# Optimization experiments

Measured on AMD Instinct MI355X. Metric: run time of the kernel, lower is better.

Reference implementation:

```python
import jax, jax.numpy as jnp
import numpy as np

N = 50000   # nodes
E = 800000  # edges (avg degree 16)
D = 64      # in_feat
OUT = 64    # out_feat


def _layernorm(x, gamma, beta, eps=1e-5):
    m = jnp.mean(x, axis=-1, keepdims=True)
    v = jnp.mean((x - m) ** 2, axis=-1, keepdims=True)  # biased var, as torch LayerNorm
    return (x - m) * jax.lax.rsqrt(v + eps) * gamma + beta


def setup_inputs() -> dict:
    key = jax.random.key(0)
    ks = jax.random.split(key, 6)
    s1 = 1.0 / np.sqrt(D)
    s2 = 1.0 / np.sqrt(2 * D)
    return {
        "x": jax.random.normal(ks[0], (N, D), dtype=jnp.float32),
        "edge_index": jax.random.randint(ks[1], (2, E), 0, N, dtype=jnp.int64),
        "W1a": jax.random.normal(ks[2], (D, D), dtype=jnp.float32) * s1,
        "W1b": jax.random.normal(ks[3], (D, D), dtype=jnp.float32) * s1,
        "gamma1": jnp.ones((D,), jnp.float32),
        "beta1": jnp.zeros((D,), jnp.float32),
        "w": jnp.ones((D,), jnp.float32),
        "gamma2": jnp.ones((D,), jnp.float32),
        "beta2": jnp.zeros((D,), jnp.float32),
        "W2a": jax.random.normal(ks[4], (D, 2 * D), dtype=jnp.float32) * s2,
        "W2b": jax.random.normal(ks[5], (OUT, D), dtype=jnp.float32) * s1,
    }


def reference(x, edge_index, W1a, W1b, gamma1, beta1, w, gamma2, beta2, W2a, W2b):
    row, col = edge_index[0], edge_index[1]
    n = x.shape[0]
    # gather -> MLP1 (two bias-free linears with ReLU)
    msg = x[row]                                        # [E, D]
    msg = jax.nn.relu(msg @ W1a.T) @ W1b.T              # [E, D]
    # scatter_mean over destination nodes
    s = jax.ops.segment_sum(msg, col, num_segments=n)   # [N, D]
    cnt = jax.ops.segment_sum(jnp.ones((col.shape[0],), x.dtype), col, num_segments=n)
    agg = s / jnp.maximum(cnt, 1.0)[:, None]
    agg = _layernorm(agg, gamma1, beta1)
    # repulsion + residual + LayerNorm
    fx = _layernorm(x + (x - agg) * w, gamma2, beta2)
    # concat -> MLP2
    h = jnp.concatenate([fx, agg], axis=1)              # [N, 2D]
    return jax.nn.relu(h @ W2a.T) @ W2b.T               # [N, OUT]
```

## Files before the change

### kernel.cpp

```cpp
#include <hip/hip_runtime.h>
#include <hip/hip_bf16.h>

#define NN 50000
#define NE 800000
#define CAP 48
#define BINS 784
#define BPAD 1024
#define P1B 391
#define CHUNK 2048
#define MLPB 768
#define SUPT 782

typedef short v8s __attribute__((ext_vector_type(8)));
typedef float v4f __attribute__((ext_vector_type(4)));
#define MFMA16(a, b, c) __builtin_amdgcn_mfma_f32_16x16x32_bf16(a, b, c, 0, 0, 0)

__device__ __forceinline__ float bfu2f(unsigned short u) {
    union { unsigned int i; float f; } v; v.i = ((unsigned int)u) << 16; return v.f;
}
__device__ __forceinline__ unsigned short f2bf_rne(float f) {
    union { float f; unsigned int i; } v; v.f = f;
    unsigned int x = v.i;
    unsigned int r = x + 0x7fffu + ((x >> 16) & 1u);
    return (unsigned short)(r >> 16);
}
__device__ __forceinline__ v8s fragf32(const float* p) {
    float4 u = ((const float4*)p)[0];
    float4 v = ((const float4*)p)[1];
    v8s r;
    r[0] = (short)f2bf_rne(u.x); r[1] = (short)f2bf_rne(u.y);
    r[2] = (short)f2bf_rne(u.z); r[3] = (short)f2bf_rne(u.w);
    r[4] = (short)f2bf_rne(v.x); r[5] = (short)f2bf_rne(v.y);
    r[6] = (short)f2bf_rne(v.z); r[7] = (short)f2bf_rne(v.w);
    return r;
}
__device__ __forceinline__ v8s fragbf(const unsigned short* p) {
    union { uint4 u; v8s s; } t; t.u = *((const uint4*)p); return t.s;
}
__device__ __forceinline__ v4f vzero() { v4f z; z[0]=0.f; z[1]=0.f; z[2]=0.f; z[3]=0.f; return z; }

__global__ __launch_bounds__(256) void p1fat_k(const int* __restrict__ ei,
                                               const float* __restrict__ x,
                                               const float* __restrict__ W1a,
                                               const float* __restrict__ W1b,
                                               unsigned int* __restrict__ chunkbuf,
                                               unsigned short* __restrict__ histT,
                                               unsigned short* __restrict__ y) {
    __shared__ unsigned int smem[6912];
    int t = threadIdx.x;
    if (blockIdx.x < P1B) {
        unsigned int* hcnt = smem;
        unsigned int* sst  = smem + BPAD;
        unsigned int* data = smem + 2 * BPAD;
        unsigned int* scan = data;
        int p = blockIdx.x;
        int e0 = p * CHUNK;
        int e1 = e0 + CHUNK; if (e1 > NE) e1 = NE;
        int ne = e1 - e0;
        bool i64 = ((ei[1] | ei[3] | ei[5] | ei[7]) == 0);
        for (int i = t; i < BPAD; i += 256) hcnt[i] = 0;
        __syncthreads();
        unsigned int packed[8];
#pragma unroll
        for (int i = 0; i < 8; ++i) {
            int e = e0 + t + 256 * i;
            unsigned int pk = 0xFFFFFFFFu;
            if (e < e1) {
                int col = i64 ? ei[2 * (NE + e)] : ei[NE + e];
                int row = i64 ? ei[2 * e]        : ei[e];
                pk = ((unsigned int)col << 16) | (unsigned int)row;
                atomicAdd(&hcnt[col >> 6], 1u);
            }
            packed[i] = pk;
        }
        __syncthreads();
        unsigned int v0 = hcnt[4 * t], v1 = hcnt[4 * t + 1];
        unsigned int v2 = hcnt[4 * t + 2], v3 = hcnt[4 * t + 3];
        unsigned int tsum = v0 + v1 + v2 + v3;
        scan[t] = tsum;
        __syncthreads();
        for (int off = 1; off < 256; off <<= 1) {
            unsigned int a = (t >= off) ? scan[t - off] : 0;
            __syncthreads();
            scan[t] += a;
            __syncthreads();
        }
        {
            unsigned int base = scan[t] - tsum;
            unsigned int s0 = base, s1 = base + v0, s2 = s1 + v1, s3 = s2 + v2;
            hcnt[4 * t] = s0; hcnt[4 * t + 1] = s1;
            hcnt[4 * t + 2] = s2; hcnt[4 * t + 3] = s3;
            sst[4 * t] = s0; sst[4 * t + 1] = s1;
            sst[4 * t + 2] = s2; sst[4 * t + 3] = s3;
        }
        __syncthreads();
#pragma unroll
        for (int i = 0; i < 8; ++i) {
            unsigned int pk = packed[i];
            if (pk != 0xFFFFFFFFu) {
                unsigned int pos = atomicAdd(&hcnt[pk >> 22], 1u);
                data[pos] = pk;
            }
        }
        __syncthreads();
        unsigned int* cb = chunkbuf + (size_t)p * CHUNK;
        for (int i = t; i < ne; i += 256) cb[i] = data[i];
        for (int i = t; i < BINS; i += 256)
            histT[i * P1B + p] = (unsigned short)sst[i];
        return;
    }
    unsigned short* wa  = (unsigned short*)smem;
    unsigned short* wb  = wa + 64 * 72;
    unsigned short* h1s = wb + 64 * 72;
    for (int i = t; i < 64 * 64; i += 256) {
        int r = i >> 6, c = i & 63;
        wa[r * 72 + c] = f2bf_rne(W1a[i]);
        wb[r * 72 + c] = f2bf_rne(W1b[i]);
    }
    __syncthreads();
    int w = t >> 6, l = t & 63;
    int lm = l & 15, lq = l >> 4;
    for (int st = blockIdx.x - P1B; st < SUPT; st += MLPB) {
        int nb = st * 64;
        int arow = nb + w * 16 + lm;
        int arc = arow < NN ? arow : NN - 1;
        const float* xr = x + (size_t)arc * 64;
        v8s a0 = fragf32(xr + lq * 8);
        v8s a1 = fragf32(xr + 32 + lq * 8);
        v4f acc[4];
#pragma unroll
        for (int jt = 0; jt < 4; ++jt) acc[jt] = vzero();
#pragma unroll
        for (int jt = 0; jt < 4; ++jt) {
            const unsigned short* wr = &wa[(jt * 16 + lm) * 72];
            acc[jt] = MFMA16(a0, fragbf(wr + lq * 8), acc[jt]);
            acc[jt] = MFMA16(a1, fragbf(wr + 32 + lq * 8), acc[jt]);
        }
#pragma unroll
        for (int jt = 0; jt < 4; ++jt)
#pragma unroll
            for (int r = 0; r < 4; ++r)
                h1s[(w * 16 + lq * 4 + r) * 72 + jt * 16 + lm] = f2bf_rne(fmaxf(acc[jt][r], 0.0f));
        __syncthreads();
        v8s c0 = fragbf(&h1s[(w * 16 + lm) * 72 + lq * 8]);
        v8s c1 = fragbf(&h1s[(w * 16 + lm) * 72 + 32 + lq * 8]);
        v4f acc2[4];
#pragma unroll
        for (int jt = 0; jt < 4; ++jt) acc2[jt] = vzero();
#pragma unroll
        for (int jt = 0; jt < 4; ++jt) {
            const unsigned short* wr = &wb[(jt * 16 + lm) * 72];
            acc2[jt] = MFMA16(c0, fragbf(wr + lq * 8), acc2[jt]);
            acc2[jt] = MFMA16(c1, fragbf(wr + 32 + lq * 8), acc2[jt]);
        }
#pragma unroll
        for (int jt = 0; jt < 4; ++jt)
#pragma unroll
            for (int r = 0; r < 4; ++r) {
                int n = nb + w * 16 + lq * 4 + r;
                if (n < NN) y[(size_t)n * 64 + jt * 16 + lm] = f2bf_rne(acc2[jt][r]);
            }
        __syncthreads();
    }
}

__global__ __launch_bounds__(256) void p2_k(const unsigned int* __restrict__ chunkbuf,
                                            const unsigned short* __restrict__ histT,
                                            unsigned short* __restrict__ bucket1,
                                            int* __restrict__ cnt) {
    __shared__ unsigned int cl[64];
    __shared__ unsigned short dl[64 * CAP];
    __shared__ unsigned int scan[256];
    __shared__ unsigned short sstart[P1B + 1];
    __shared__ unsigned short base[P1B + 1];
    int t = threadIdx.x;
    int b = blockIdx.x;
    int c0 = b << 6;
    for (int i = t; i < 64; i += 256) cl[i] = 0;
    for (int i = t; i < 64 * CAP / 2; i += 256) ((unsigned int*)dl)[i] = 0;
    unsigned int l0 = 0, l1 = 0;
    {
        int s0 = 2 * t, s1 = 2 * t + 1;
        if (s0 < P1B) {
            unsigned int st = histT[b * P1B + s0];
            int ne = NE - s0 * CHUNK; if (ne > CHUNK) ne = CHUNK;
            unsigned int en = (b == BINS - 1) ? (unsigned int)ne : histT[(b + 1) * P1B + s0];
            l0 = en - st;
            sstart[s0] = (unsigned short)st;
        }
        if (s1 < P1B) {
            unsigned int st = histT[b * P1B + s1];
            int ne = NE - s1 * CHUNK; if (ne > CHUNK) ne = CHUNK;
            unsigned int en = (b == BINS - 1) ? (unsigned int)ne : histT[(b + 1) * P1B + s1];
            l1 = en - st;
            sstart[s1] = (unsigned short)st;
        }
    }
    unsigned int psum = l0 + l1;
    scan[t] = psum;
    __syncthreads();
    for (int off = 1; off < 256; off <<= 1) {
        unsigned int a = (t >= off) ? scan[t - off] : 0;
        __syncthreads();
        scan[t] += a;
        __syncthreads();
    }
    {
        unsigned int excl = scan[t] - psum;
        if (2 * t < P1B)     base[2 * t]     = (unsigned short)excl;
        if (2 * t + 1 < P1B) base[2 * t + 1] = (unsigned short)(excl + l0);
    }
    __syncthreads();
    int tot = (int)scan[255];
    for (int k = t; k < tot; k += 256) {
        int lo = 0, hi = P1B - 1;
#pragma unroll
        for (int it = 0; it < 9; ++it) {
            int mid = (lo + hi + 1) >> 1;
            if ((int)base[mid] <= k) lo = mid; else hi = mid - 1;
        }
        int idx = (int)sstart[lo] + (k - (int)base[lo]);
        unsigned int d = chunkbuf[(size_t)lo * CHUNK + idx];
        int c = (int)(d >> 16) - c0;
        unsigned int slot = atomicAdd(&cl[c], 1u);
        if (slot < CAP) dl[c * CAP + slot] = (unsigned short)(d & 0xffffu);
    }
    __syncthreads();
    for (int i = t; i < 64; i += 256)
        if (c0 + i < NN) cnt[c0 + i] = (int)cl[i];
    uint4* dst = (uint4*)(bucket1 + (size_t)c0 * CAP);
    const uint4* src = (const uint4*)dl;
    for (int i = t; i < 64 * CAP / 8; i += 256) dst[i] = src[i];
}

__device__ __forceinline__ float wsum64(float v) {
#pragma unroll
    for (int o = 32; o > 0; o >>= 1) v += __shfl_xor(v, o, 64);
    return v;
}
__device__ __forceinline__ void ln_store(float s0, float s1, int tdeg, int n, int p, int j, int f0,
                                         const float* __restrict__ x,
                                         const float* __restrict__ g1, const float* __restrict__ b1,
                                         const float* __restrict__ wrep,
                                         const float* __restrict__ g2, const float* __restrict__ b2,
                                         unsigned short* __restrict__ h) {
    float inv = 1.0f / (float)(tdeg > 1 ? tdeg : 1);
    float a0 = s0 * inv, a1 = s1 * inv;
    float m = wsum64(a0 + a1) * (1.0f / 128.0f);
    float d0 = a0 - m, d1 = a1 - m;
    float var = wsum64(d0 * d0 + d1 * d1) * (1.0f / 128.0f);
    float r = rsqrtf(var + 1e-5f);
    float2 g1v = *(const float2*)(g1 + f0);
    float2 b1v = *(const float2*)(b1 + f0);
    a0 = d0 * r * g1v.x + b1v.x;
    a1 = d1 * r * g1v.y + b1v.y;
    float2 xv = *(const float2*)(x + (size_t)n * 64 + f0);
    float2 wv = *(const float2*)(wrep + f0);
    float t0 = xv.x + (xv.x - a0) * wv.x;
    float t1 = xv.y + (xv.y - a1) * wv.y;
    float m2 = wsum64(t0 + t1) * (1.0f / 128.0f);
    float e0 = t0 - m2, e1 = t1 - m2;
    float var2 = wsum64(e0 * e0 + e1 * e1) * (1.0f / 128.0f);
    float r2 = rsqrtf(var2 + 1e-5f);
    float2 g2v = *(const float2*)(g2 + f0);
    float2 b2v = *(const float2*)(b2 + f0);
    float fx0 = e0 * r2 * g2v.x + b2v.x;
    float fx1 = e1 * r2 * g2v.y + b2v.y;
    unsigned* hw = (unsigned*)(h + (size_t)n * 128);
    if (p == 0) hw[j]      = (unsigned)f2bf_rne(fx0) | ((unsigned)f2bf_rne(fx1) << 16);
    else        hw[32 + j] = (unsigned)f2bf_rne(a0)  | ((unsigned)f2bf_rne(a1)  << 16);
}
__global__ __launch_bounds__(256) void gathernorm_k(const int* __restrict__ cnt,
                                                    const unsigned short* __restrict__ bucket1,
                                                    const unsigned short* __restrict__ y,
                                                    const float* __restrict__ x,
                                                    const float* __restrict__ g1, const float* __restrict__ b1,
                                                    const float* __restrict__ wrep,
                                                    const float* __restrict__ g2, const float* __restrict__ b2,
                                                    unsigned short* __restrict__ h) {
    int n0 = blockIdx.x * 8 + (threadIdx.x >> 6) * 2;
    if (n0 >= NN) return;
    int n1 = n0 + 1;
    int n1c = n1 < NN ? n1 : n0;
    int l = threadIdx.x & 63;
    int p = l >> 5;
    int j = l & 31;
    int f0 = 2 * j;
    int dA = cnt[n0], dB = cnt[n1c];
    int eA = dA < CAP ? dA : CAP;
    int eB = dB < CAP ? dB : CAP;
    const uint4* bpA = (const uint4*)(bucket1 + (size_t)n0 * CAP);
    const uint4* bpB = (const uint4*)(bucket1 + (size_t)n1c * CAP);
    uint4 qA[6], qB[6];
#pragma unroll
    for (int i = 0; i < 6; ++i) { qA[i] = bpA[i]; qB[i] = bpB[i]; }
    float sA0 = 0.f, sA1 = 0.f, sB0 = 0.f, sB1 = 0.f;
#pragma unroll
    for (int c = 0; c < 6; ++c) {
        bool cA = c * 8 < eA, cB = c * 8 < eB;
        if (cA | cB) {
            unsigned wA[4] = { qA[c].x, qA[c].y, qA[c].z, qA[c].w };
            unsigned wB[4] = { qB[c].x, qB[c].y, qB[c].z, qB[c].w };
#pragma unroll
            for (int i = 0; i < 4; ++i) {
                int e = c * 8 + 2 * i + p;
                int idA = (int)((wA[i] >> (p * 16)) & 0xffffu);
                int idB = (int)((wB[i] >> (p * 16)) & 0xffffu);
                unsigned uA = *(const unsigned*)(y + (size_t)idA * 64 + f0);
                unsigned uB = *(const unsigned*)(y + (size_t)idB * 64 + f0);
                bool okA = cA && e < eA, okB = cB && e < eB;
                sA0 += okA ? bfu2f((unsigned short)(uA & 0xffffu)) : 0.0f;
                sA1 += okA ? bfu2f((unsigned short)(uA >> 16)) : 0.0f;
                sB0 += okB ? bfu2f((unsigned short)(uB & 0xffffu)) : 0.0f;
                sB1 += okB ? bfu2f((unsigned short)(uB >> 16)) : 0.0f;
            }
        }
    }
    sA0 += __shfl_xor(sA0, 32, 64);
    sA1 += __shfl_xor(sA1, 32, 64);
    sB0 += __shfl_xor(sB0, 32, 64);
    sB1 += __shfl_xor(sB1, 32, 64);
    ln_store(sA0, sA1, dA, n0, p, j, f0, x, g1, b1, wrep, g2, b2, h);
    if (n1 < NN)
        ln_store(sB0, sB1, dB, n1, p, j, f0, x, g1, b1, wrep, g2, b2, h);
}

__global__ __launch_bounds__(256) void mlp2_k(const unsigned short* hin,
                                              const float* __restrict__ W2a,
                                              const float* __restrict__ W2b,
                                              float* out) {
    __shared__ unsigned short sm2[64 * 136 + 64 * 72 + 64 * 72];
    unsigned short* wa2 = sm2;
    unsigned short* wb2 = wa2 + 64 * 136;
    unsigned short* t2s = wb2 + 64 * 72;
    int t = threadIdx.x;
    for (int i = t; i < 64 * 128; i += 256) {
        int r = i >> 7, c = i & 127;
        wa2[r * 136 + c] = f2bf_rne(W2a[i]);
    }
    for (int i = t; i < 64 * 64; i += 256) {
        int r = i >> 6, c = i & 63;
        wb2[r * 72 + c] = f2bf_rne(W2b[i]);
    }
    __syncthreads();
    int w = t >> 6, l = t & 63;
    int lm = l & 15, lq = l >> 4;
    for (int st = blockIdx.x; st < SUPT; st += MLPB) {
        int nb = st * 64;
        int arow = nb + w * 16 + lm;
        int arc = arow < NN ? arow : NN - 1;
        const unsigned short* fr = hin + (size_t)arc * 128;
        v8s a0 = fragbf(fr + lq * 8);
        v8s a1 = fragbf(fr + 32 + lq * 8);
        v8s a2 = fragbf(fr + 64 + lq * 8);
        v8s a3 = fragbf(fr + 96 + lq * 8);
        v4f acc[4];
#pragma unroll
        for (int jt = 0; jt < 4; ++jt) acc[jt] = vzero();
#pragma unroll
        for (int jt = 0; jt < 4; ++jt) {
            const unsigned short* wr = &wa2[(jt * 16 + lm) * 136];
            acc[jt] = MFMA16(a0, fragbf(wr + lq * 8), acc[jt]);
            acc[jt] = MFMA16(a1, fragbf(wr + 32 + lq * 8), acc[jt]);
            acc[jt] = MFMA16(a2, fragbf(wr + 64 + lq * 8), acc[jt]);
            acc[jt] = MFMA16(a3, fragbf(wr + 96 + lq * 8), acc[jt]);
        }
#pragma unroll
        for (int jt = 0; jt < 4; ++jt)
#pragma unroll
            for (int r = 0; r < 4; ++r)
                t2s[(w * 16 + lq * 4 + r) * 72 + jt * 16 + lm] = f2bf_rne(fmaxf(acc[jt][r], 0.0f));
        __syncthreads();
        v8s c0 = fragbf(&t2s[(w * 16 + lm) * 72 + lq * 8]);
        v8s c1 = fragbf(&t2s[(w * 16 + lm) * 72 + 32 + lq * 8]);
        v4f acc2[4];
#pragma unroll
        for (int jt = 0; jt < 4; ++jt) acc2[jt] = vzero();
#pragma unroll
        for (int jt = 0; jt < 4; ++jt) {
            const unsigned short* wr = &wb2[(jt * 16 + lm) * 72];
            acc2[jt] = MFMA16(c0, fragbf(wr + lq * 8), acc2[jt]);
            acc2[jt] = MFMA16(c1, fragbf(wr + 32 + lq * 8), acc2[jt]);
        }
#pragma unroll
        for (int jt = 0; jt < 4; ++jt)
#pragma unroll
            for (int r = 0; r < 4; ++r) {
                int n = nb + w * 16 + lq * 4 + r;
                if (n < NN) out[(size_t)n * 64 + jt * 16 + lm] = acc2[jt][r];
            }
        __syncthreads();
    }
}

extern "C" void kernel_launch(void* const* d_in, const int* in_sizes, int n_in,
                              void* d_out, int out_size, void* d_ws, size_t ws_size,
                              hipStream_t stream) {
    const float* x   = (const float*)d_in[0];
    const int*   ei  = (const int*)d_in[1];
    const float* W1a = (const float*)d_in[2];
    const float* W1b = (const float*)d_in[3];
    const float* g1  = (const float*)d_in[4];
    const float* b1  = (const float*)d_in[5];
    const float* w   = (const float*)d_in[6];
    const float* g2  = (const float*)d_in[7];
    const float* b2  = (const float*)d_in[8];
    const float* W2a = (const float*)d_in[9];
    const float* W2b = (const float*)d_in[10];

    char* ws = (char*)d_ws;
    unsigned short* y        = (unsigned short*)(ws + 0);
    unsigned int*   chunkbuf = (unsigned int*)(ws + 6400000);
    unsigned short* histT    = (unsigned short*)(ws + 9603072);
    unsigned short* bucket1  = (unsigned short*)(ws + 10216160);
    int*            cnt      = (int*)(ws + 15033056);

    p1fat_k<<<P1B + MLPB, 256, 0, stream>>>(ei, x, W1a, W1b, chunkbuf, histT, y);
    p2_k<<<BINS, 256, 0, stream>>>(chunkbuf, histT, bucket1, cnt);
    gathernorm_k<<<(NN + 7) / 8, 256, 0, stream>>>(cnt, bucket1, y, x,
                                                   g1, b1, w, g2, b2, (unsigned short*)d_out);
    mlp2_k<<<MLPB, 256, 0, stream>>>((const unsigned short*)d_out, W2a, W2b, (float*)d_out);
    (void)in_sizes; (void)n_in; (void)out_size; (void)ws_size;
}
```

Baseline: 138.7 us.

## Fuse bucket scatter, gather-normalize and MLP2 into one kernel over 16-node bins

Shrinks the histogram bins from 64 to 16 destination nodes (3125 bins, bank-padded in shared memory) and transposes histT to a per-chunk row layout. Merges p2_k, gathernorm_k and mlp2_k into a single kernel in which each block buckets its 16 nodes' edges into shared memory, gathers and layer-normalizes them, and runs the MLP2 MFMAs directly from LDS. This removes two launches and the global round-trips through bucket1/cnt and the bf16 h buffer. In exchange every block re-converts the full W2a/W2b weights to bf16 and runs a per-block scan over all 391 chunks, across about four times as many blocks.

```diff
diff --git a/kernel.cpp b/kernel.cpp
--- a/kernel.cpp
+++ b/kernel.cpp
@@ -4,12 +4,13 @@
 #define NN 50000
 #define NE 800000
 #define CAP 48
-#define BINS 784
-#define BPAD 1024
+#define BINS 3125
+#define HROW 3126
 #define P1B 391
 #define CHUNK 2048
 #define MLPB 768
 #define SUPT 782
+#define HIDX(b) ((b) + ((b) >> 4))
 
 typedef short v8s __attribute__((ext_vector_type(8)));
 typedef float v4f __attribute__((ext_vector_type(4)));
@@ -46,19 +47,19 @@
                                                unsigned int* __restrict__ chunkbuf,
                                                unsigned short* __restrict__ histT,
                                                unsigned short* __restrict__ y) {
-    __shared__ unsigned int smem[6912];
+    __shared__ __align__(16) unsigned int smem[8448];
     int t = threadIdx.x;
     if (blockIdx.x < P1B) {
-        unsigned int* hcnt = smem;
-        unsigned int* sst  = smem + BPAD;
-        unsigned int* data = smem + 2 * BPAD;
-        unsigned int* scan = data;
-        int p = blockIdx.x;
-        int e0 = p * CHUNK;
+        unsigned int*   hcnt  = smem;
+        unsigned short* sst16 = (unsigned short*)(smem + 4352);
+        unsigned int*   data  = smem + 4352 + 2048;
+        unsigned int*   scan  = data;
+        int pc = blockIdx.x;
+        int e0 = pc * CHUNK;
         int e1 = e0 + CHUNK; if (e1 > NE) e1 = NE;
         int ne = e1 - e0;
         bool i64 = ((ei[1] | ei[3] | ei[5] | ei[7]) == 0);
-        for (int i = t; i < BPAD; i += 256) hcnt[i] = 0;
+        for (int i = t; i < 4352; i += 256) hcnt[i] = 0;
         __syncthreads();
         unsigned int packed[8];
 #pragma unroll
@@ -69,14 +70,14 @@
                 int col = i64 ? ei[2 * (NE + e)] : ei[NE + e];
                 int row = i64 ? ei[2 * e]        : ei[e];
                 pk = ((unsigned int)col << 16) | (unsigned int)row;
-                atomicAdd(&hcnt[col >> 6], 1u);
+                atomicAdd(&hcnt[HIDX(col >> 4)], 1u);
             }
             packed[i] = pk;
         }
         __syncthreads();
-        unsigned int v0 = hcnt[4 * t], v1 = hcnt[4 * t + 1];
-        unsigned int v2 = hcnt[4 * t + 2], v3 = hcnt[4 * t + 3];
-        unsigned int tsum = v0 + v1 + v2 + v3;
+        unsigned int vv[16], tsum = 0;
+#pragma unroll
+        for (int k = 0; k < 16; ++k) { vv[k] = hcnt[HIDX(16 * t + k)]; tsum += vv[k]; }
         scan[t] = tsum;
         __syncthreads();
         for (int off = 1; off < 256; off <<= 1) {
@@ -86,27 +87,30 @@
             __syncthreads();
         }
         {
-            unsigned int base = scan[t] - tsum;
-            unsigned int s0 = base, s1 = base + v0, s2 = s1 + v1, s3 = s2 + v2;
-            hcnt[4 * t] = s0; hcnt[4 * t + 1] = s1;
-            hcnt[4 * t + 2] = s2; hcnt[4 * t + 3] = s3;
-            sst[4 * t] = s0; sst[4 * t + 1] = s1;
-            sst[4 * t + 2] = s2; sst[4 * t + 3] = s3;
+            unsigned int run = scan[t] - tsum;
+#pragma unroll
+            for (int k = 0; k < 16; ++k) {
+                int bb = 16 * t + k;
+                hcnt[HIDX(bb)] = run;
+                sst16[bb] = (unsigned short)run;
+                run += vv[k];
+            }
         }
         __syncthreads();
 #pragma unroll
         for (int i = 0; i < 8; ++i) {
             unsigned int pk = packed[i];
             if (pk != 0xFFFFFFFFu) {
-                unsigned int pos = atomicAdd(&hcnt[pk >> 22], 1u);
+                unsigned int pos = atomicAdd(&hcnt[HIDX(pk >> 20)], 1u);
                 data[pos] = pk;
             }
         }
         __syncthreads();
-        unsigned int* cb = chunkbuf + (size_t)p * CHUNK;
+        unsigned int* cb = chunkbuf + (size_t)pc * CHUNK;
         for (int i = t; i < ne; i += 256) cb[i] = data[i];
-        for (int i = t; i < BINS; i += 256)
-            histT[i * P1B + p] = (unsigned short)sst[i];
+        unsigned short* hrow = histT + (size_t)pc * HROW;
+        for (int i = t; i < BINS; i += 256) hrow[i] = sst16[i];
+        if (t == 0) hrow[BINS] = (unsigned short)ne;
         return;
     }
     unsigned short* wa  = (unsigned short*)smem;
@@ -164,75 +168,6 @@
     }
 }
 
-__global__ __launch_bounds__(256) void p2_k(const unsigned int* __restrict__ chunkbuf,
-                                            const unsigned short* __restrict__ histT,
-                                            unsigned short* __restrict__ bucket1,
-                                            int* __restrict__ cnt) {
-    __shared__ unsigned int cl[64];
-    __shared__ unsigned short dl[64 * CAP];
-    __shared__ unsigned int scan[256];
-    __shared__ unsigned short sstart[P1B + 1];
-    __shared__ unsigned short base[P1B + 1];
-    int t = threadIdx.x;
-    int b = blockIdx.x;
-    int c0 = b << 6;
-    for (int i = t; i < 64; i += 256) cl[i] = 0;
-    for (int i = t; i < 64 * CAP / 2; i += 256) ((unsigned int*)dl)[i] = 0;
-    unsigned int l0 = 0, l1 = 0;
-    {
-        int s0 = 2 * t, s1 = 2 * t + 1;
-        if (s0 < P1B) {
-            unsigned int st = histT[b * P1B + s0];
-            int ne = NE - s0 * CHUNK; if (ne > CHUNK) ne = CHUNK;
-            unsigned int en = (b == BINS - 1) ? (unsigned int)ne : histT[(b + 1) * P1B + s0];
-            l0 = en - st;
-            sstart[s0] = (unsigned short)st;
-        }
-        if (s1 < P1B) {
-            unsigned int st = histT[b * P1B + s1];
-            int ne = NE - s1 * CHUNK; if (ne > CHUNK) ne = CHUNK;
-            unsigned int en = (b == BINS - 1) ? (unsigned int)ne : histT[(b + 1) * P1B + s1];
-            l1 = en - st;
-            sstart[s1] = (unsigned short)st;
-        }
-    }
-    unsigned int psum = l0 + l1;
-    scan[t] = psum;
-    __syncthreads();
-    for (int off = 1; off < 256; off <<= 1) {
-        unsigned int a = (t >= off) ? scan[t - off] : 0;
-        __syncthreads();
-        scan[t] += a;
-        __syncthreads();
-    }
-    {
-        unsigned int excl = scan[t] - psum;
-        if (2 * t < P1B)     base[2 * t]     = (unsigned short)excl;
-        if (2 * t + 1 < P1B) base[2 * t + 1] = (unsigned short)(excl + l0);
-    }
-    __syncthreads();
-    int tot = (int)scan[255];
-    for (int k = t; k < tot; k += 256) {
-        int lo = 0, hi = P1B - 1;
-#pragma unroll
-        for (int it = 0; it < 9; ++it) {
-            int mid = (lo + hi + 1) >> 1;
-            if ((int)base[mid] <= k) lo = mid; else hi = mid - 1;
-        }
-        int idx = (int)sstart[lo] + (k - (int)base[lo]);
-        unsigned int d = chunkbuf[(size_t)lo * CHUNK + idx];
-        int c = (int)(d >> 16) - c0;
-        unsigned int slot = atomicAdd(&cl[c], 1u);
-        if (slot < CAP) dl[c * CAP + slot] = (unsigned short)(d & 0xffffu);
-    }
-    __syncthreads();
-    for (int i = t; i < 64; i += 256)
-        if (c0 + i < NN) cnt[c0 + i] = (int)cl[i];
-    uint4* dst = (uint4*)(bucket1 + (size_t)c0 * CAP);
-    const uint4* src = (const uint4*)dl;
-    for (int i = t; i < 64 * CAP / 8; i += 256) dst[i] = src[i];
-}
-
 __device__ __forceinline__ float wsum64(float v) {
 #pragma unroll
     for (int o = 32; o > 0; o >>= 1) v += __shfl_xor(v, o, 64);
@@ -243,7 +178,7 @@
                                          const float* __restrict__ g1, const float* __restrict__ b1,
                                          const float* __restrict__ wrep,
                                          const float* __restrict__ g2, const float* __restrict__ b2,
-                                         unsigned short* __restrict__ h) {
+                                         unsigned short* hrow) {
     float inv = 1.0f / (float)(tdeg > 1 ? tdeg : 1);
     float a0 = s0 * inv, a1 = s1 * inv;
     float m = wsum64(a0 + a1) * (1.0f / 128.0f);
@@ -266,74 +201,34 @@
     float2 b2v = *(const float2*)(b2 + f0);
     float fx0 = e0 * r2 * g2v.x + b2v.x;
     float fx1 = e1 * r2 * g2v.y + b2v.y;
-    unsigned* hw = (unsigned*)(h + (size_t)n * 128);
+    unsigned* hw = (unsigned*)hrow;
     if (p == 0) hw[j]      = (unsigned)f2bf_rne(fx0) | ((unsigned)f2bf_rne(fx1) << 16);
     else        hw[32 + j] = (unsigned)f2bf_rne(a0)  | ((unsigned)f2bf_rne(a1)  << 16);
 }
-__global__ __launch_bounds__(256) void gathernorm_k(const int* __restrict__ cnt,
-                                                    const unsigned short* __restrict__ bucket1,
-                                                    const unsigned short* __restrict__ y,
-                                                    const float* __restrict__ x,
-                                                    const float* __restrict__ g1, const float* __restrict__ b1,
-                                                    const float* __restrict__ wrep,
-                                                    const float* __restrict__ g2, const float* __restrict__ b2,
-                                                    unsigned short* __restrict__ h) {
-    int n0 = blockIdx.x * 8 + (threadIdx.x >> 6) * 2;
-    if (n0 >= NN) return;
-    int n1 = n0 + 1;
-    int n1c = n1 < NN ? n1 : n0;
-    int l = threadIdx.x & 63;
-    int p = l >> 5;
-    int j = l & 31;
-    int f0 = 2 * j;
-    int dA = cnt[n0], dB = cnt[n1c];
-    int eA = dA < CAP ? dA : CAP;
-    int eB = dB < CAP ? dB : CAP;
-    const uint4* bpA = (const uint4*)(bucket1 + (size_t)n0 * CAP);
-    const uint4* bpB = (const uint4*)(bucket1 + (size_t)n1c * CAP);
-    uint4 qA[6], qB[6];
-#pragma unroll
-    for (int i = 0; i < 6; ++i) { qA[i] = bpA[i]; qB[i] = bpB[i]; }
-    float sA0 = 0.f, sA1 = 0.f, sB0 = 0.f, sB1 = 0.f;
-#pragma unroll
-    for (int c = 0; c < 6; ++c) {
-        bool cA = c * 8 < eA, cB = c * 8 < eB;
-        if (cA | cB) {
-            unsigned wA[4] = { qA[c].x, qA[c].y, qA[c].z, qA[c].w };
-            unsigned wB[4] = { qB[c].x, qB[c].y, qB[c].z, qB[c].w };
-#pragma unroll
-            for (int i = 0; i < 4; ++i) {
-                int e = c * 8 + 2 * i + p;
-                int idA = (int)((wA[i] >> (p * 16)) & 0xffffu);
-                int idB = (int)((wB[i] >> (p * 16)) & 0xffffu);
-                unsigned uA = *(const unsigned*)(y + (size_t)idA * 64 + f0);
-                unsigned uB = *(const unsigned*)(y + (size_t)idB * 64 + f0);
-                bool okA = cA && e < eA, okB = cB && e < eB;
-                sA0 += okA ? bfu2f((unsigned short)(uA & 0xffffu)) : 0.0f;
-                sA1 += okA ? bfu2f((unsigned short)(uA >> 16)) : 0.0f;
-                sB0 += okB ? bfu2f((unsigned short)(uB & 0xffffu)) : 0.0f;
-                sB1 += okB ? bfu2f((unsigned short)(uB >> 16)) : 0.0f;
-            }
-        }
-    }
-    sA0 += __shfl_xor(sA0, 32, 64);
-    sA1 += __shfl_xor(sA1, 32, 64);
-    sB0 += __shfl_xor(sB0, 32, 64);
-    sB1 += __shfl_xor(sB1, 32, 64);
-    ln_store(sA0, sA1, dA, n0, p, j, f0, x, g1, b1, wrep, g2, b2, h);
-    if (n1 < NN)
-        ln_store(sB0, sB1, dB, n1, p, j, f0, x, g1, b1, wrep, g2, b2, h);
-}
-
-__global__ __launch_bounds__(256) void mlp2_k(const unsigned short* hin,
+
+__global__ __launch_bounds__(256) void p2gm_k(const unsigned int* __restrict__ chunkbuf,
+                                              const unsigned short* __restrict__ histT,
+                                              const unsigned short* __restrict__ y,
+                                              const float* __restrict__ x,
+                                              const float* __restrict__ g1, const float* __restrict__ b1,
+                                              const float* __restrict__ wrep,
+                                              const float* __restrict__ g2, const float* __restrict__ b2,
                                               const float* __restrict__ W2a,
                                               const float* __restrict__ W2b,
-                                              float* out) {
-    __shared__ unsigned short sm2[64 * 136 + 64 * 72 + 64 * 72];
-    unsigned short* wa2 = sm2;
+                                              float* __restrict__ out) {
+    __shared__ __align__(16) unsigned int k2s[9368];
+    unsigned short* wa2 = (unsigned short*)k2s;
     unsigned short* wb2 = wa2 + 64 * 136;
     unsigned short* t2s = wb2 + 64 * 72;
+    unsigned short* hs  = t2s + 16 * 72;
+    unsigned short* dl  = hs + 16 * 136;
+    unsigned int*   cl     = k2s + 8704;
+    unsigned int*   scan   = cl + 16;
+    unsigned short* sstart = (unsigned short*)(scan + 256);
+    unsigned short* sbase  = sstart + 392;
     int t = threadIdx.x;
+    int b = blockIdx.x;
+    int n0g = b * 16;
     for (int i = t; i < 64 * 128; i += 256) {
         int r = i >> 7, c = i & 127;
         wa2[r * 136 + c] = f2bf_rne(W2a[i]);
@@ -342,55 +237,113 @@
         int r = i >> 6, c = i & 63;
         wb2[r * 72 + c] = f2bf_rne(W2b[i]);
     }
+    if (t < 16) cl[t] = 0;
+    for (int i = t; i < 16 * CAP / 2; i += 256) ((unsigned int*)dl)[i] = 0;
+    unsigned l0 = 0, l1 = 0;
+    int s0 = 2 * t, s1 = 2 * t + 1;
+    if (s0 < P1B) {
+        unsigned st = histT[(size_t)s0 * HROW + b], en = histT[(size_t)s0 * HROW + b + 1];
+        l0 = en - st; sstart[s0] = (unsigned short)st;
+    }
+    if (s1 < P1B) {
+        unsigned st = histT[(size_t)s1 * HROW + b], en = histT[(size_t)s1 * HROW + b + 1];
+        l1 = en - st; sstart[s1] = (unsigned short)st;
+    }
+    unsigned psum = l0 + l1;
+    scan[t] = psum;
+    __syncthreads();
+    for (int off = 1; off < 256; off <<= 1) {
+        unsigned a = (t >= off) ? scan[t - off] : 0;
+        __syncthreads();
+        scan[t] += a;
+        __syncthreads();
+    }
+    {
+        unsigned excl = scan[t] - psum;
+        if (s0 < P1B) sbase[s0] = (unsigned short)excl;
+        if (s1 < P1B) sbase[s1] = (unsigned short)(excl + l0);
+    }
+    __syncthreads();
+    int tot = (int)scan[255];
+    for (int k = t; k < tot; k += 256) {
+        int lo = 0, hi = P1B - 1;
+#pragma unroll
+        for (int it = 0; it < 9; ++it) {
+            int mid = (lo + hi + 1) >> 1;
+            if ((int)sbase[mid] <= k) lo = mid; else hi = mid - 1;
+        }
+        int idx = (int)sstart[lo] + (k - (int)sbase[lo]);
+        unsigned d = chunkbuf[(size_t)lo * CHUNK + idx];
+        int c = (int)(d >> 16) - n0g;
+        unsigned slot = atomicAdd(&cl[c], 1u);
+        if (slot < CAP) dl[c * CAP + slot] = (unsigned short)(d & 0xffffu);
+    }
     __syncthreads();
     int w = t >> 6, l = t & 63;
+    int p = l >> 5, j = l & 31, f0 = 2 * j;
+#pragma unroll
+    for (int q = 0; q < 2; ++q) {
+        int nl0 = q * 8 + w * 2, nl1 = nl0 + 1;
+        int dA = (int)cl[nl0], dB = (int)cl[nl1];
+        int eA = dA < CAP ? dA : CAP;
+        int eB = dB < CAP ? dB : CAP;
+        float sA0 = 0.f, sA1 = 0.f, sB0 = 0.f, sB1 = 0.f;
+#pragma unroll
+        for (int c6 = 0; c6 < 6; ++c6) {
+            bool cA = c6 * 8 < eA, cB = c6 * 8 < eB;
+            if (cA | cB) {
+#pragma unroll
+                for (int i = 0; i < 4; ++i) {
+                    int e = c6 * 8 + 2 * i + p;
+                    int idA = (int)dl[nl0 * CAP + e];
+                    int idB = (int)dl[nl1 * CAP + e];
+                    unsigned uA = *(const unsigned*)(y + (size_t)idA * 64 + f0);
+                    unsigned uB = *(const unsigned*)(y + (size_t)idB * 64 + f0);
+                    bool okA = cA && e < eA, okB = cB && e < eB;
+                    sA0 += okA ? bfu2f((unsigned short)(uA & 0xffffu)) : 0.0f;
+                    sA1 += okA ? bfu2f((unsigned short)(uA >> 16)) : 0.0f;
+                    sB0 += okB ? bfu2f((unsigned short)(uB & 0xffffu)) : 0.0f;
+                    sB1 += okB ? bfu2f((unsigned short)(uB >> 16)) : 0.0f;
+                }
+            }
+        }
+        sA0 += __shfl_xor(sA0, 32, 64);
+        sA1 += __shfl_xor(sA1, 32, 64);
+        sB0 += __shfl_xor(sB0, 32, 64);
+        sB1 += __shfl_xor(sB1, 32, 64);
+        ln_store(sA0, sA1, dA, n0g + nl0, p, j, f0, x, g1, b1, wrep, g2, b2, hs + nl0 * 136);
+        ln_store(sB0, sB1, dB, n0g + nl1, p, j, f0, x, g1, b1, wrep, g2, b2, hs + nl1 * 136);
+    }
+    __syncthreads();
     int lm = l & 15, lq = l >> 4;
-    for (int st = blockIdx.x; st < SUPT; st += MLPB) {
-        int nb = st * 64;
-        int arow = nb + w * 16 + lm;
-        int arc = arow < NN ? arow : NN - 1;
-        const unsigned short* fr = hin + (size_t)arc * 128;
-        v8s a0 = fragbf(fr + lq * 8);
-        v8s a1 = fragbf(fr + 32 + lq * 8);
-        v8s a2 = fragbf(fr + 64 + lq * 8);
-        v8s a3 = fragbf(fr + 96 + lq * 8);
-        v4f acc[4];
-#pragma unroll
-        for (int jt = 0; jt < 4; ++jt) acc[jt] = vzero();
-#pragma unroll
-        for (int jt = 0; jt < 4; ++jt) {
-            const unsigned short* wr = &wa2[(jt * 16 + lm) * 136];
-            acc[jt] = MFMA16(a0, fragbf(wr + lq * 8), acc[jt]);
-            acc[jt] = MFMA16(a1, fragbf(wr + 32 + lq * 8), acc[jt]);
-            acc[jt] = MFMA16(a2, fragbf(wr + 64 + lq * 8), acc[jt]);
-            acc[jt] = MFMA16(a3, fragbf(wr + 96 + lq * 8), acc[jt]);
-        }
-#pragma unroll
-        for (int jt = 0; jt < 4; ++jt)
-#pragma unroll
-            for (int r = 0; r < 4; ++r)
-                t2s[(w * 16 + lq * 4 + r) * 72 + jt * 16 + lm] = f2bf_rne(fmaxf(acc[jt][r], 0.0f));
-        __syncthreads();
-        v8s c0 = fragbf(&t2s[(w * 16 + lm) * 72 + lq * 8]);
-        v8s c1 = fragbf(&t2s[(w * 16 + lm) * 72 + 32 + lq * 8]);
-        v4f acc2[4];
-#pragma unroll
-        for (int jt = 0; jt < 4; ++jt) acc2[jt] = vzero();
-#pragma unroll
-        for (int jt = 0; jt < 4; ++jt) {
-            const unsigned short* wr = &wb2[(jt * 16 + lm) * 72];
-            acc2[jt] = MFMA16(c0, fragbf(wr + lq * 8), acc2[jt]);
-            acc2[jt] = MFMA16(c1, fragbf(wr + 32 + lq * 8), acc2[jt]);
-        }
-#pragma unroll
-        for (int jt = 0; jt < 4; ++jt)
-#pragma unroll
-            for (int r = 0; r < 4; ++r) {
-                int n = nb + w * 16 + lq * 4 + r;
-                if (n < NN) out[(size_t)n * 64 + jt * 16 + lm] = acc2[jt][r];
-            }
-        __syncthreads();
-    }
+    const unsigned short* fr = hs + lm * 136;
+    v8s a0 = fragbf(fr + lq * 8);
+    v8s a1 = fragbf(fr + 32 + lq * 8);
+    v8s a2 = fragbf(fr + 64 + lq * 8);
+    v8s a3 = fragbf(fr + 96 + lq * 8);
+    v4f acc = vzero();
+    {
+        const unsigned short* wr = &wa2[(w * 16 + lm) * 136];
+        acc = MFMA16(a0, fragbf(wr + lq * 8), acc);
+        acc = MFMA16(a1, fragbf(wr + 32 + lq * 8), acc);
+        acc = MFMA16(a2, fragbf(wr + 64 + lq * 8), acc);
+        acc = MFMA16(a3, fragbf(wr + 96 + lq * 8), acc);
+    }
+#pragma unroll
+    for (int r = 0; r < 4; ++r)
+        t2s[(lq * 4 + r) * 72 + w * 16 + lm] = f2bf_rne(fmaxf(acc[r], 0.0f));
+    __syncthreads();
+    v8s c0f = fragbf(&t2s[lm * 72 + lq * 8]);
+    v8s c1f = fragbf(&t2s[lm * 72 + 32 + lq * 8]);
+    v4f acc2 = vzero();
+    {
+        const unsigned short* wr = &wb2[(w * 16 + lm) * 72];
+        acc2 = MFMA16(c0f, fragbf(wr + lq * 8), acc2);
+        acc2 = MFMA16(c1f, fragbf(wr + 32 + lq * 8), acc2);
+    }
+#pragma unroll
+    for (int r = 0; r < 4; ++r)
+        out[(size_t)(n0g + lq * 4 + r) * 64 + w * 16 + lm] = acc2[r];
 }
 
 extern "C" void kernel_launch(void* const* d_in, const int* in_sizes, int n_in,
@@ -412,13 +365,9 @@
     unsigned short* y        = (unsigned short*)(ws + 0);
     unsigned int*   chunkbuf = (unsigned int*)(ws + 6400000);
     unsigned short* histT    = (unsigned short*)(ws + 9603072);
-    unsigned short* bucket1  = (unsigned short*)(ws + 10216160);
-    int*            cnt      = (int*)(ws + 15033056);
 
     p1fat_k<<<P1B + MLPB, 256, 0, stream>>>(ei, x, W1a, W1b, chunkbuf, histT, y);
-    p2_k<<<BINS, 256, 0, stream>>>(chunkbuf, histT, bucket1, cnt);
-    gathernorm_k<<<(NN + 7) / 8, 256, 0, stream>>>(cnt, bucket1, y, x,
-                                                   g1, b1, w, g2, b2, (unsigned short*)d_out);
-    mlp2_k<<<MLPB, 256, 0, stream>>>((const unsigned short*)d_out, W2a, W2b, (float*)d_out);
+    p2gm_k<<<BINS, 256, 0, stream>>>(chunkbuf, histT, y, x, g1, b1, w, g2, b2,
+                                     W2a, W2b, (float*)d_out);
     (void)in_sizes; (void)n_in; (void)out_size; (void)ws_size;
 }
```

After: 152.5 us. 10.0% more time.
